# Optimization experiments

Measured on AMD Instinct MI355X. Metric: run time of the kernel, lower is better.

The kernel has to match this reference:

```python
import jax, jax.numpy as jnp
import numpy as np
import math

B, S, D, E, H = 8, 384, 768, 768, 12
HD = E // H
MAXL = 512

def _xavier(key, shape):
    fan_in, fan_out = shape[1], shape[0]
    lim = math.sqrt(6.0 / (fan_in + fan_out))
    return jax.random.uniform(key, shape, jnp.float32, -lim, lim)

def setup_inputs() -> dict:
    key = jax.random.key(0)
    ks = jax.random.split(key, 12)
    return {
        "x": jax.random.normal(ks[0], (B, S, D), jnp.float32),
        "mask": jnp.ones((B, S), jnp.int32),
        "segment_ids": jax.random.randint(ks[1], (B, S), 0, 2).astype(jnp.int32),
        "sep_distances": jax.random.normal(ks[2], (B, S), jnp.float32),
        "Wq": _xavier(ks[3], (E, D)), "bq": jnp.zeros((E,), jnp.float32),
        "Wk": _xavier(ks[4], (E, D)), "bk": jnp.zeros((E,), jnp.float32),
        "Wv": _xavier(ks[5], (E, D)), "bv": jnp.zeros((E,), jnp.float32),
        "rel_emb": jax.random.normal(ks[6], (2 * MAXL - 1, D), jnp.float32),
        "Wpk": _xavier(ks[7], (E, D)), "bpk": jnp.zeros((E,), jnp.float32),
        "Wpq": _xavier(ks[8], (E, D)), "bpq": jnp.zeros((E,), jnp.float32),
        "same_bias": jnp.zeros((H,), jnp.float32),
        "cross_bias": jnp.zeros((H,), jnp.float32),
        "sep_scale": jnp.full((H,), 0.25, jnp.float32),
        "sep_decay": jnp.full((H,), 0.35, jnp.float32),
        "Wo": _xavier(ks[9], (D, E)), "bo": jnp.zeros((D,), jnp.float32),
    }

def reference(x, mask, segment_ids, sep_distances, Wq, bq, Wk, bk, Wv, bv,
              rel_emb, Wpk, bpk, Wpq, bpq, same_bias, cross_bias,
              sep_scale, sep_decay, Wo, bo):
    b, s, _ = x.shape
    def shape_heads(t):  # [b,s,E] -> [b,H,s,HD]
        return t.reshape(b, s, H, HD).transpose(0, 2, 1, 3)
    q = shape_heads(x @ Wq.T + bq)
    k = shape_heads(x @ Wk.T + bk)
    v = shape_heads(x @ Wv.T + bv)
    # relative positions i - j, clamped and shifted
    rel_pos = jnp.arange(s)[:, None] - jnp.arange(s)[None, :]
    rel_pos = jnp.clip(rel_pos, -(MAXL - 1), MAXL - 1) + (MAXL - 1)
    rel = rel_emb[rel_pos]                     # [s,s,D]
    pos_k = (rel @ Wpk.T + bpk).reshape(s, s, H, HD)  # [i,j,h,d]
    pos_q = (rel @ Wpq.T + bpq).reshape(s, s, H, HD)
    c2c = jnp.einsum('bhid,bhjd->bhij', q, k)
    c2p = jnp.einsum('bhid,ijhd->bhij', q, pos_k)
    p2c = jnp.einsum('ijhd,bhjd->bhij', pos_q, k)
    logits = (c2c + c2p + p2c) / math.sqrt(HD * 3.0)
    # segment bias
    same = (segment_ids[:, :, None] == segment_ids[:, None, :]).astype(jnp.float32)[:, None]  # [b,1,s,s]
    cross = 1.0 - same
    hb = lambda p: p[None, :, None, None]
    seg_bias = same * hb(same_bias) + cross * hb(cross_bias)
    abs_sep = jnp.abs(sep_distances)
    gap = jnp.abs(abs_sep[:, :, None] - abs_sep[:, None, :])[:, None]  # [b,1,s,s]
    decay = jax.nn.softplus(sep_decay)[None, :, None, None] + 1e-4
    seg_bias = seg_bias + cross * jnp.exp(-gap * decay) * hb(sep_scale)
    logits = logits + seg_bias
    # mask: [b,s] -> [b,1,1,s]
    m = mask[:, None, None, :]
    logits = jnp.where(m == 0, jnp.float32(-9e15), logits)
    attn = jax.nn.softmax(logits, axis=-1)
    vals = jnp.einsum('bhij,bhjd->bhid', attn, v)
    vals = vals.transpose(0, 2, 1, 3).reshape(b, s, E)
    return vals @ Wo.T + bo
```

## Files before the change

### kernel.cpp

```cpp
#include <hip/hip_runtime.h>
#include <math.h>

#define B_  8
#define S_  384
#define H_  12
#define HD_ 64
#define E_  768
#define D_  768

typedef float  floatx4 __attribute__((ext_vector_type(4)));
typedef __bf16 bf16x8  __attribute__((ext_vector_type(8)));
typedef unsigned int ux4 __attribute__((ext_vector_type(4)));

__device__ __forceinline__ unsigned short f2bf(float f) {
    union { float f; unsigned u; } x; x.f = f;
    unsigned r = x.u + 0x7fff + ((x.u >> 16) & 1);
    return (unsigned short)(r >> 16);
}
__device__ __forceinline__ float bf2f(unsigned short u) {
    union { unsigned u; float f; } x; x.u = ((unsigned)u) << 16;
    return x.f;
}
__device__ __forceinline__ bf16x8 gld8(const unsigned short* p) {
    return __builtin_bit_cast(bf16x8, *(const ux4*)p);
}
__device__ __forceinline__ int tadr(int row, int cD) {
    return (row * 8 + (cD ^ (row & 7))) * 8;
}
__device__ __forceinline__ bf16x8 lds8(const unsigned short* base, int row, int cD) {
    return __builtin_bit_cast(bf16x8, *(const ux4*)(base + tadr(row, cD)));
}

__global__ __launch_bounds__(256) void convert_all(
    const float* __restrict__ x,
    const float* __restrict__ Wq, const float* __restrict__ Wk,
    const float* __restrict__ Wv, const float* __restrict__ Wo,
    const float* __restrict__ Wpk, const float* __restrict__ Wpq,
    const float* __restrict__ rel128,
    unsigned short* __restrict__ xb,
    unsigned short* __restrict__ wqb, unsigned short* __restrict__ wkb,
    unsigned short* __restrict__ wvb, unsigned short* __restrict__ wob,
    unsigned short* __restrict__ wpkb, unsigned short* __restrict__ wpqb,
    unsigned short* __restrict__ relb)
{
    const int seg = blockIdx.y;
    const int e = (blockIdx.x * 256 + threadIdx.x) * 4;
    const float* src;
    unsigned short* dst;
    if (seg < 4)       { src = x + (size_t)seg * 589824; dst = xb + (size_t)seg * 589824; }
    else if (seg == 4) { src = Wq;  dst = wqb; }
    else if (seg == 5) { src = Wk;  dst = wkb; }
    else if (seg == 6) { src = Wv;  dst = wvb; }
    else if (seg == 7) { src = Wo;  dst = wob; }
    else if (seg == 8) { src = Wpk; dst = wpkb; }
    else if (seg == 9) { src = Wpq; dst = wpqb; }
    else               { src = rel128; dst = relb; }

    float4 v;
    if (seg == 10 && e >= 767 * 768) v = make_float4(0.f, 0.f, 0.f, 0.f);
    else                             v = *(const float4*)(src + e);
    ushort4 o;
    o.x = f2bf(v.x); o.y = f2bf(v.y); o.z = f2bf(v.z); o.w = f2bf(v.w);
    *(ushort4*)(dst + e) = o;
}

__global__ __launch_bounds__(256) void proj_all(
    const unsigned short* __restrict__ xb, const unsigned short* __restrict__ relb,
    const unsigned short* __restrict__ wq, const unsigned short* __restrict__ wk,
    const unsigned short* __restrict__ wv, const unsigned short* __restrict__ wpk,
    const unsigned short* __restrict__ wpq,
    const float* __restrict__ bq, const float* __restrict__ bk,
    const float* __restrict__ bv, const float* __restrict__ bpk,
    const float* __restrict__ bpq,
    unsigned short* __restrict__ qb, unsigned short* __restrict__ kb,
    unsigned short* __restrict__ vtb, unsigned short* __restrict__ pkb,
    unsigned short* __restrict__ pqb)
{
    const int bid = blockIdx.x;
    int z, mt, nt;
    if (bid < 864) {
        z = bid / 288; const int r = bid - z * 288; mt = r / 6; nt = r - mt * 6;
    } else {
        const int r2 = bid - 864; z = 3 + r2 / 72;
        const int r = r2 % 72; mt = r / 6; nt = r - mt * 6;
    }
    const int m0 = mt * 64, n0 = nt * 128;

    const unsigned short* A = (z < 3) ? xb : relb;
    const unsigned short* W = (z == 0) ? wq : (z == 1) ? wk : (z == 2) ? wv
                            : (z == 3) ? wpk : wpq;
    const float* bias = (z == 0) ? bq : (z == 1) ? bk : (z == 2) ? bv
                      : (z == 3) ? bpk : bpq;
    unsigned short* C = (z == 0) ? qb : (z == 1) ? kb : (z == 2) ? vtb
                      : (z == 3) ? pkb : pqb;

    __shared__ unsigned short As[64 * 64];
    __shared__ unsigned short Ws[128 * 64];

    const int tid  = threadIdx.x;
    const int lane = tid & 63;
    const int wv_  = tid >> 6;
    const int quad = lane >> 4, l16 = lane & 15;

    floatx4 acc[4][2];
#pragma unroll
    for (int i = 0; i < 4; ++i)
#pragma unroll
        for (int j = 0; j < 2; ++j) acc[i][j] = (floatx4){0.f, 0.f, 0.f, 0.f};

    for (int k0 = 0; k0 < 768; k0 += 64) {
        __syncthreads();
#pragma unroll
        for (int r = 0; r < 2; ++r) {
            const int idx = tid + 256 * r;
            const int row = idx >> 3, cL = idx & 7, cD = cL ^ (row & 7);
            __builtin_amdgcn_global_load_lds(
                (__attribute__((address_space(1))) void*)(A + (size_t)(m0 + row) * 768 + k0 + cD * 8),
                (__attribute__((address_space(3))) void*)&As[idx * 8], 16, 0, 0);
        }
#pragma unroll
        for (int r = 0; r < 4; ++r) {
            const int idx = tid + 256 * r;
            const int row = idx >> 3, cL = idx & 7, cD = cL ^ (row & 7);
            __builtin_amdgcn_global_load_lds(
                (__attribute__((address_space(1))) void*)(W + (size_t)(n0 + row) * 768 + k0 + cD * 8),
                (__attribute__((address_space(3))) void*)&Ws[idx * 8], 16, 0, 0);
        }
        __syncthreads();

        bf16x8 a[4][2], b[2][2];
#pragma unroll
        for (int mi = 0; mi < 4; ++mi)
#pragma unroll
            for (int kc = 0; kc < 2; ++kc)
                a[mi][kc] = lds8(As, mi * 16 + l16, kc * 4 + quad);
#pragma unroll
        for (int ni = 0; ni < 2; ++ni)
#pragma unroll
            for (int kc = 0; kc < 2; ++kc)
                b[ni][kc] = lds8(Ws, wv_ * 32 + ni * 16 + l16, kc * 4 + quad);
#pragma unroll
        for (int mi = 0; mi < 4; ++mi)
#pragma unroll
            for (int ni = 0; ni < 2; ++ni)
#pragma unroll
                for (int kc = 0; kc < 2; ++kc)
                    acc[mi][ni] = __builtin_amdgcn_mfma_f32_16x16x32_bf16(
                        a[mi][kc], b[ni][kc], acc[mi][ni], 0, 0, 0);
    }

#pragma unroll
    for (int ni = 0; ni < 2; ++ni) {
        const int n = n0 + wv_ * 32 + ni * 16 + l16;
        const float bn = bias[n];
#pragma unroll
        for (int mi = 0; mi < 4; ++mi) {
            const int mbase = m0 + mi * 16 + quad * 4;
            if (z == 2) {
                const int bb = mbase / S_, s = mbase - bb * S_;
                const int h = n >> 6, hd = n & 63;
                ushort4 o;
                o.x = f2bf(acc[mi][ni][0] + bn);
                o.y = f2bf(acc[mi][ni][1] + bn);
                o.z = f2bf(acc[mi][ni][2] + bn);
                o.w = f2bf(acc[mi][ni][3] + bn);
                *(ushort4*)&C[(((size_t)(bb * H_ + h) << 6) + hd) * S_ + s] = o;
            } else if (z < 2) {
#pragma unroll
                for (int reg = 0; reg < 4; ++reg) {
                    const int m = mbase + reg;
                    const int bb = m / S_, s = m - bb * S_;
                    const int h = n >> 6, hd = n & 63;
                    C[(((size_t)(bb * H_ + h) * S_ + s) << 6) + hd] =
                        f2bf(acc[mi][ni][reg] + bn);
                }
            } else {
#pragma unroll
                for (int reg = 0; reg < 4; ++reg)
                    C[(size_t)(mbase + reg) * 768 + n] = f2bf(acc[mi][ni][reg] + bn);
            }
        }
    }
}

__global__ __launch_bounds__(256) void gemm_out(
    const unsigned short* __restrict__ A, const unsigned short* __restrict__ W,
    const float* __restrict__ bias, float* __restrict__ C)
{
    const int mt = blockIdx.x / 6, nt = blockIdx.x - mt * 6;
    const int m0 = mt * 64, n0 = nt * 128;

    __shared__ unsigned short As[64 * 64];
    __shared__ unsigned short Ws[128 * 64];

    const int tid  = threadIdx.x;
    const int lane = tid & 63;
    const int wv_  = tid >> 6;
    const int quad = lane >> 4, l16 = lane & 15;

    floatx4 acc[4][2];
#pragma unroll
    for (int i = 0; i < 4; ++i)
#pragma unroll
        for (int j = 0; j < 2; ++j) acc[i][j] = (floatx4){0.f, 0.f, 0.f, 0.f};

    for (int k0 = 0; k0 < 768; k0 += 64) {
        __syncthreads();
#pragma unroll
        for (int r = 0; r < 2; ++r) {
            const int idx = tid + 256 * r;
            const int row = idx >> 3, cL = idx & 7, cD = cL ^ (row & 7);
            __builtin_amdgcn_global_load_lds(
                (__attribute__((address_space(1))) void*)(A + (size_t)(m0 + row) * 768 + k0 + cD * 8),
                (__attribute__((address_space(3))) void*)&As[idx * 8], 16, 0, 0);
        }
#pragma unroll
        for (int r = 0; r < 4; ++r) {
            const int idx = tid + 256 * r;
            const int row = idx >> 3, cL = idx & 7, cD = cL ^ (row & 7);
            __builtin_amdgcn_global_load_lds(
                (__attribute__((address_space(1))) void*)(W + (size_t)(n0 + row) * 768 + k0 + cD * 8),
                (__attribute__((address_space(3))) void*)&Ws[idx * 8], 16, 0, 0);
        }
        __syncthreads();

        bf16x8 a[4][2], b[2][2];
#pragma unroll
        for (int mi = 0; mi < 4; ++mi)
#pragma unroll
            for (int kc = 0; kc < 2; ++kc)
                a[mi][kc] = lds8(As, mi * 16 + l16, kc * 4 + quad);
#pragma unroll
        for (int ni = 0; ni < 2; ++ni)
#pragma unroll
            for (int kc = 0; kc < 2; ++kc)
                b[ni][kc] = lds8(Ws, wv_ * 32 + ni * 16 + l16, kc * 4 + quad);
#pragma unroll
        for (int mi = 0; mi < 4; ++mi)
#pragma unroll
            for (int ni = 0; ni < 2; ++ni)
#pragma unroll
                for (int kc = 0; kc < 2; ++kc)
                    acc[mi][ni] = __builtin_amdgcn_mfma_f32_16x16x32_bf16(
                        a[mi][kc], b[ni][kc], acc[mi][ni], 0, 0, 0);
    }

#pragma unroll
    for (int ni = 0; ni < 2; ++ni) {
        const int n = n0 + wv_ * 32 + ni * 16 + l16;
        const float bn = bias[n];
#pragma unroll
        for (int mi = 0; mi < 4; ++mi)
#pragma unroll
            for (int reg = 0; reg < 4; ++reg) {
                const int m = m0 + mi * 16 + quad * 4 + reg;
                C[(size_t)m * 768 + n] = acc[mi][ni][reg] + bn;
            }
    }
}

__global__ __launch_bounds__(256) void attn_mfma(
    const unsigned short* __restrict__ qg, const unsigned short* __restrict__ kg,
    const unsigned short* __restrict__ vtg,
    const unsigned short* __restrict__ pkg, const unsigned short* __restrict__ pqg,
    const int* __restrict__ seg, const float* __restrict__ sep,
    const int* __restrict__ mask,
    const float* __restrict__ same_bias, const float* __restrict__ cross_bias,
    const float* __restrict__ sep_scale, const float* __restrict__ sep_decay,
    unsigned short* __restrict__ part_O, float* __restrict__ part_ml)
{
    __shared__ unsigned short Ks [64 * 64];
    __shared__ unsigned short Vts[64 * 64];
    __shared__ unsigned short PKs[128 * 64];
    __shared__ unsigned short PQs[128 * 64];
    __shared__ float CP[64 * 68];

    const int tid  = threadIdx.x;
    const int lane = tid & 63, w = tid >> 6;
    const int l16  = lane & 15, quad = lane >> 4;
    const int ty = tid >> 4, tx = tid & 15;
    const int it = blockIdx.x, h = blockIdx.y;
    const int b  = blockIdx.z / 6, jt = blockIdx.z - 6 * b;
    const int i0 = it * 64, j0 = jt * 64;
    const size_t bh = (size_t)(b * H_ + h);

    const unsigned short* kbase  = kg  + bh * S_ * 64;
    const unsigned short* vtbase = vtg + bh * 64 * S_;
    const int dbase = i0 - j0 + 320;

    bf16x8 qf[2];
#pragma unroll
    for (int ks = 0; ks < 2; ++ks)
        qf[ks] = gld8(qg + (bh * S_ + i0 + 16 * w + l16) * 64 + ks * 32 + quad * 8);

#pragma unroll
    for (int r = 0; r < 2; ++r) {
        const int idx = tid + 256 * r;
        const int row = idx >> 3, cL = idx & 7;
        const int cD = cL ^ (row & 7);
        __builtin_amdgcn_global_load_lds(
            (__attribute__((address_space(1))) void*)(kbase + (size_t)(j0 + row) * 64 + cD * 8),
            (__attribute__((address_space(3))) void*)&Ks[idx * 8], 16, 0, 0);
        __builtin_amdgcn_global_load_lds(
            (__attribute__((address_space(1))) void*)(vtbase + (size_t)row * S_ + j0 + cD * 8),
            (__attribute__((address_space(3))) void*)&Vts[idx * 8], 16, 0, 0);
    }
#pragma unroll
    for (int r = 0; r < 4; ++r) {
        const int idx = tid + 256 * r;
        const int row = idx >> 3, cL = idx & 7;
        const int cD = cL ^ (row & 7);
        const size_t go = (size_t)(dbase + row) * 768 + h * 64 + cD * 8;
        __builtin_amdgcn_global_load_lds(
            (__attribute__((address_space(1))) void*)(pkg + go),
            (__attribute__((address_space(3))) void*)&PKs[idx * 8], 16, 0, 0);
        __builtin_amdgcn_global_load_lds(
            (__attribute__((address_space(1))) void*)(pqg + go),
            (__attribute__((address_space(3))) void*)&PQs[idx * 8], 16, 0, 0);
    }

    float ai_r[4]; int si_r[4];
#pragma unroll
    for (int p = 0; p < 4; ++p) {
        const int ii = 4 * ty + p;
        ai_r[p] = fabsf(sep[b * S_ + i0 + ii]);
        si_r[p] = seg[b * S_ + i0 + ii];
    }

    const float sb  = same_bias[h];
    const float cb  = cross_bias[h];
    const float ssc = sep_scale[h];
    const float sd  = sep_decay[h];
    const float dec = fmaxf(sd, 0.f) + log1pf(__expf(-fabsf(sd))) + 1e-4f;
    const float isc = 0.07216878364870323f;

    __syncthreads();

    bf16x8 kf[4][2];
#pragma unroll
    for (int nj = 0; nj < 4; ++nj)
#pragma unroll
        for (int ks = 0; ks < 2; ++ks)
            kf[nj][ks] = lds8(Ks, 16 * nj + l16, ks * 4 + quad);

#pragma unroll
    for (int nj = 0; nj < 4; ++nj) {
        floatx4 acc = (floatx4){0.f, 0.f, 0.f, 0.f};
#pragma unroll
        for (int ks = 0; ks < 2; ++ks)
            acc = __builtin_amdgcn_mfma_f32_16x16x32_bf16(qf[ks], kf[nj][ks], acc, 0, 0, 0);
#pragma unroll
        for (int reg = 0; reg < 4; ++reg) {
            const int ii = 16 * w + quad * 4 + reg;
            CP[ii * 68 + 16 * nj + l16] = acc[reg];
        }
    }

#pragma unroll
    for (int f = 0; f < 5; ++f) {
        const int nd = w + f;
        floatx4 acc = (floatx4){0.f, 0.f, 0.f, 0.f};
#pragma unroll
        for (int ks = 0; ks < 2; ++ks) {
            bf16x8 bf = lds8(PKs, 16 * nd + l16, ks * 4 + quad);
            acc = __builtin_amdgcn_mfma_f32_16x16x32_bf16(qf[ks], bf, acc, 0, 0, 0);
        }
        const int ddloc = 16 * nd + l16;
#pragma unroll
        for (int reg = 0; reg < 4; ++reg) {
            const int ii = 16 * w + quad * 4 + reg;
            const int jj = ii - ddloc + 63;
            if (jj >= 0 && jj < 64)
                CP[ii * 68 + jj] += acc[reg];
        }
    }

#pragma unroll
    for (int f = 0; f < 5; ++f) {
        const int nd = w + f;
        bf16x8 pqf[2];
#pragma unroll
        for (int ks = 0; ks < 2; ++ks)
            pqf[ks] = lds8(PQs, 16 * nd + l16, ks * 4 + quad);
#pragma unroll
        for (int g = 0; g < 2; ++g) {
            const int nj = (g == 0) ? (3 - f) : (4 - f);
            if (nj < 0 || nj > 3) continue;
            floatx4 acc = (floatx4){0.f, 0.f, 0.f, 0.f};
#pragma unroll
            for (int ks = 0; ks < 2; ++ks)
                acc = __builtin_amdgcn_mfma_f32_16x16x32_bf16(pqf[ks], kf[nj][ks], acc, 0, 0, 0);
            const int jj = 16 * nj + l16;
#pragma unroll
            for (int reg = 0; reg < 4; ++reg) {
                const int ddloc = 16 * nd + quad * 4 + reg;
                const int ii = ddloc + jj - 63;
                if (ii >= 16 * w && ii < 16 * w + 16)
                    CP[ii * 68 + jj] += acc[reg];
            }
        }
    }

    unsigned short* Pp = (unsigned short*)CP;
    float* pml = part_ml + (size_t)(jt * 576 + ((b * H_ + h) * 6 + it)) * 128;
#pragma unroll
    for (int p = 0; p < 4; ++p) {
        const int ii = 4 * ty + p;
        const float aii = ai_r[p];
        const int   sii = si_r[p];
        float lg[4];
        float tmax = -INFINITY;
#pragma unroll
        for (int r = 0; r < 4; ++r) {
            const int jl = 4 * tx + r;
            float xv = CP[ii * 68 + jl] * isc;
            const float ajv = fabsf(sep[b * S_ + j0 + jl]);
            const int   sjv = seg[b * S_ + j0 + jl];
            const float gap = fabsf(aii - ajv);
            const float bias = (sii == sjv) ? sb
                             : cb + __expf(-gap * dec) * ssc;
            xv += bias;
            if (mask[b * S_ + j0 + jl] == 0) xv = -9.0e15f;
            lg[r] = xv;
            tmax = fmaxf(tmax, xv);
        }
#pragma unroll
        for (int off = 1; off < 16; off <<= 1)
            tmax = fmaxf(tmax, __shfl_xor(tmax, off));
        float rs = 0.f;
        ushort4 pw;
#pragma unroll
        for (int r = 0; r < 4; ++r) {
            const float e = __expf(lg[r] - tmax);
            rs += e;
            ((unsigned short*)&pw)[r] = f2bf(e);
        }
#pragma unroll
        for (int off = 1; off < 16; off <<= 1)
            rs += __shfl_xor(rs, off);
        if (tx == 0) {
            pml[ii]      = tmax;
            pml[64 + ii] = rs;
        }
        *(ushort4*)&Pp[ii * 136 + 4 * tx] = pw;
    }

    bf16x8 pA[2];
#pragma unroll
    for (int ks = 0; ks < 2; ++ks)
        pA[ks] = __builtin_bit_cast(bf16x8,
            *(const ux4*)&Pp[(16 * w + l16) * 136 + ks * 32 + quad * 8]);
    floatx4 O[4];
#pragma unroll
    for (int nd = 0; nd < 4; ++nd) {
        O[nd] = (floatx4){0.f, 0.f, 0.f, 0.f};
#pragma unroll
        for (int ks = 0; ks < 2; ++ks) {
            bf16x8 bf = lds8(Vts, 16 * nd + l16, ks * 4 + quad);
            O[nd] = __builtin_amdgcn_mfma_f32_16x16x32_bf16(pA[ks], bf, O[nd], 0, 0, 0);
        }
    }

    unsigned short* pO = part_O + (size_t)(jt * 576 + ((b * H_ + h) * 6 + it)) * 4096;
#pragma unroll
    for (int nd = 0; nd < 4; ++nd) {
        const int d = 16 * nd + l16;
#pragma unroll
        for (int reg = 0; reg < 4; ++reg) {
            const int ii = 16 * w + quad * 4 + reg;
            pO[ii * 64 + d] = f2bf(O[nd][reg]);
        }
    }
}

__global__ __launch_bounds__(256) void merge_attn(
    const unsigned short* __restrict__ part_O, const float* __restrict__ part_ml,
    unsigned short* __restrict__ vals)
{
    const int idx = blockIdx.x;
    const int b  = idx / (H_ * 6);
    const int r  = idx - b * H_ * 6;
    const int h  = r / 6, it = r - h * 6;
    const int tid = threadIdx.x;
    const int ii = tid >> 2, c = (tid & 3) * 16;

    float m[6], l[6];
#pragma unroll
    for (int jc = 0; jc < 6; ++jc) {
        const float* pml = part_ml + (size_t)(jc * 576 + idx) * 128;
        m[jc] = pml[ii];
        l[jc] = pml[64 + ii];
    }
    float M = m[0];
#pragma unroll
    for (int jc = 1; jc < 6; ++jc) M = fmaxf(M, m[jc]);
    float wsum = 0.f, wc[6];
#pragma unroll
    for (int jc = 0; jc < 6; ++jc) {
        wc[jc] = __expf(m[jc] - M);
        wsum += wc[jc] * l[jc];
    }
    const float inv = (wsum > 0.f) ? 1.f / wsum : 0.f;

    float o[16];
#pragma unroll
    for (int e = 0; e < 16; ++e) o[e] = 0.f;
#pragma unroll
    for (int jc = 0; jc < 6; ++jc) {
        const unsigned short* pO = part_O + ((size_t)(jc * 576 + idx)) * 4096
                                 + ii * 64 + c;
        ux4 u0 = *(const ux4*)pO;
        ux4 u1 = *(const ux4*)(pO + 8);
        const unsigned short* us0 = (const unsigned short*)&u0;
        const unsigned short* us1 = (const unsigned short*)&u1;
#pragma unroll
        for (int e = 0; e < 8; ++e) {
            o[e]     += wc[jc] * bf2f(us0[e]);
            o[8 + e] += wc[jc] * bf2f(us1[e]);
        }
    }
    ushort4 w0, w1, w2, w3;
#pragma unroll
    for (int e = 0; e < 4; ++e) {
        ((unsigned short*)&w0)[e] = f2bf(o[e] * inv);
        ((unsigned short*)&w1)[e] = f2bf(o[4 + e] * inv);
        ((unsigned short*)&w2)[e] = f2bf(o[8 + e] * inv);
        ((unsigned short*)&w3)[e] = f2bf(o[12 + e] * inv);
    }
    unsigned short* dst = vals + ((size_t)(b * S_ + it * 64 + ii)) * E_ + h * 64 + c;
    *(ushort4*)(dst)      = w0;
    *(ushort4*)(dst + 4)  = w1;
    *(ushort4*)(dst + 8)  = w2;
    *(ushort4*)(dst + 12) = w3;
}

extern "C" void kernel_launch(void* const* d_in, const int* in_sizes, int n_in,
                              void* d_out, int out_size, void* d_ws, size_t ws_size,
                              hipStream_t stream)
{
    const float* x         = (const float*)d_in[0];
    const int*   mask      = (const int*)d_in[1];
    const int*   seg       = (const int*)d_in[2];
    const float* sep       = (const float*)d_in[3];
    const float* Wq        = (const float*)d_in[4];
    const float* bq        = (const float*)d_in[5];
    const float* Wk        = (const float*)d_in[6];
    const float* bk        = (const float*)d_in[7];
    const float* Wv        = (const float*)d_in[8];
    const float* bv        = (const float*)d_in[9];
    const float* rel_emb   = (const float*)d_in[10];
    const float* Wpk       = (const float*)d_in[11];
    const float* bpk       = (const float*)d_in[12];
    const float* Wpq       = (const float*)d_in[13];
    const float* bpq       = (const float*)d_in[14];
    const float* same_bias = (const float*)d_in[15];
    const float* cross_bias= (const float*)d_in[16];
    const float* sep_scale = (const float*)d_in[17];
    const float* sep_decay = (const float*)d_in[18];
    const float* Wo        = (const float*)d_in[19];
    const float* bo        = (const float*)d_in[20];

    const size_t QKVN = (size_t)B_ * S_ * E_;
    const size_t WN   = (size_t)768 * 768;

    unsigned short* xb    = (unsigned short*)d_ws;
    unsigned short* wqb   = xb   + QKVN;
    unsigned short* wkb   = wqb  + WN;
    unsigned short* wvb   = wkb  + WN;
    unsigned short* wob   = wvb  + WN;
    unsigned short* wpkb  = wob  + WN;
    unsigned short* wpqb  = wpkb + WN;
    unsigned short* relb  = wpqb + WN;
    unsigned short* qb    = relb + WN;
    unsigned short* kb    = qb   + QKVN;
    unsigned short* vtb   = kb   + QKVN;
    unsigned short* pkb   = vtb  + QKVN;
    unsigned short* pqb   = pkb  + WN;
    unsigned short* valsb = pqb  + WN;
    unsigned short* partO = valsb + QKVN;
    float*          partml= (float*)(partO + (size_t)6 * 576 * 4096);

    convert_all<<<dim3(576, 11), 256, 0, stream>>>(
        x, Wq, Wk, Wv, Wo, Wpk, Wpq, rel_emb + (size_t)128 * D_,
        xb, wqb, wkb, wvb, wob, wpkb, wpqb, relb);

    proj_all<<<dim3(1008), 256, 0, stream>>>(
        xb, relb, wqb, wkb, wvb, wpkb, wpqb,
        bq, bk, bv, bpk, bpq, qb, kb, vtb, pkb, pqb);

    attn_mfma<<<dim3(6, 12, 48), 256, 0, stream>>>(
        qb, kb, vtb, pkb, pqb, seg, sep, mask,
        same_bias, cross_bias, sep_scale, sep_decay, partO, partml);

    merge_attn<<<dim3(576), 256, 0, stream>>>(partO, partml, valsb);

    gemm_out<<<dim3(288), 256, 0, stream>>>(valsb, wob, bo, (float*)d_out);
}
```

Before: 211.4 us.

## Load attention MFMA operands directly from global memory instead of staging in LDS

Drops the LDS staging buffers for K, V^T and the positional key/query tiles. MFMA fragments are now read straight from global memory, which also removes the block-wide barrier. The j-side sep, segment and mask values are loaded into registers once before the softmax loop, and the kernel asks for 4 blocks per CU via launch bounds. The aim is to cut LDS use and allow higher occupancy, at the cost of less coalesced and partly redundant global loads that depend on L1/L2 hits.

```diff
diff --git a/kernel.cpp b/kernel.cpp
--- a/kernel.cpp
+++ b/kernel.cpp
@@ -259,7 +259,7 @@
     }
 }
 
-__global__ __launch_bounds__(256) void attn_mfma(
+__global__ __launch_bounds__(256, 4) void attn_mfma(
     const unsigned short* __restrict__ qg, const unsigned short* __restrict__ kg,
     const unsigned short* __restrict__ vtg,
     const unsigned short* __restrict__ pkg, const unsigned short* __restrict__ pqg,
@@ -269,10 +269,6 @@
     const float* __restrict__ sep_scale, const float* __restrict__ sep_decay,
     unsigned short* __restrict__ part_O, float* __restrict__ part_ml)
 {
-    __shared__ unsigned short Ks [64 * 64];
-    __shared__ unsigned short Vts[64 * 64];
-    __shared__ unsigned short PKs[128 * 64];
-    __shared__ unsigned short PQs[128 * 64];
     __shared__ float CP[64 * 68];
 
     const int tid  = threadIdx.x;
@@ -293,31 +289,13 @@
     for (int ks = 0; ks < 2; ++ks)
         qf[ks] = gld8(qg + (bh * S_ + i0 + 16 * w + l16) * 64 + ks * 32 + quad * 8);
 
-#pragma unroll
-    for (int r = 0; r < 2; ++r) {
-        const int idx = tid + 256 * r;
-        const int row = idx >> 3, cL = idx & 7;
-        const int cD = cL ^ (row & 7);
-        __builtin_amdgcn_global_load_lds(
-            (__attribute__((address_space(1))) void*)(kbase + (size_t)(j0 + row) * 64 + cD * 8),
-            (__attribute__((address_space(3))) void*)&Ks[idx * 8], 16, 0, 0);
-        __builtin_amdgcn_global_load_lds(
-            (__attribute__((address_space(1))) void*)(vtbase + (size_t)row * S_ + j0 + cD * 8),
-            (__attribute__((address_space(3))) void*)&Vts[idx * 8], 16, 0, 0);
-    }
-#pragma unroll
-    for (int r = 0; r < 4; ++r) {
-        const int idx = tid + 256 * r;
-        const int row = idx >> 3, cL = idx & 7;
-        const int cD = cL ^ (row & 7);
-        const size_t go = (size_t)(dbase + row) * 768 + h * 64 + cD * 8;
-        __builtin_amdgcn_global_load_lds(
-            (__attribute__((address_space(1))) void*)(pkg + go),
-            (__attribute__((address_space(3))) void*)&PKs[idx * 8], 16, 0, 0);
-        __builtin_amdgcn_global_load_lds(
-            (__attribute__((address_space(1))) void*)(pqg + go),
-            (__attribute__((address_space(3))) void*)&PQs[idx * 8], 16, 0, 0);
-    }
+    bf16x8 kf[4][2];
+#pragma unroll
+    for (int nj = 0; nj < 4; ++nj)
+#pragma unroll
+        for (int ks = 0; ks < 2; ++ks)
+            kf[nj][ks] = gld8(kbase + (size_t)(j0 + 16 * nj + l16) * 64
+                              + ks * 32 + quad * 8);
 
     float ai_r[4]; int si_r[4];
 #pragma unroll
@@ -325,6 +303,14 @@
         const int ii = 4 * ty + p;
         ai_r[p] = fabsf(sep[b * S_ + i0 + ii]);
         si_r[p] = seg[b * S_ + i0 + ii];
+    }
+    float aj_r[4]; int sj_r[4], mk_r[4];
+#pragma unroll
+    for (int r = 0; r < 4; ++r) {
+        const int jl = 4 * tx + r;
+        aj_r[r] = fabsf(sep[b * S_ + j0 + jl]);
+        sj_r[r] = seg[b * S_ + j0 + jl];
+        mk_r[r] = mask[b * S_ + j0 + jl];
     }
 
     const float sb  = same_bias[h];
@@ -334,15 +320,6 @@
     const float dec = fmaxf(sd, 0.f) + log1pf(__expf(-fabsf(sd))) + 1e-4f;
     const float isc = 0.07216878364870323f;
 
-    __syncthreads();
-
-    bf16x8 kf[4][2];
-#pragma unroll
-    for (int nj = 0; nj < 4; ++nj)
-#pragma unroll
-        for (int ks = 0; ks < 2; ++ks)
-            kf[nj][ks] = lds8(Ks, 16 * nj + l16, ks * 4 + quad);
-
 #pragma unroll
     for (int nj = 0; nj < 4; ++nj) {
         floatx4 acc = (floatx4){0.f, 0.f, 0.f, 0.f};
@@ -362,7 +339,8 @@
         floatx4 acc = (floatx4){0.f, 0.f, 0.f, 0.f};
 #pragma unroll
         for (int ks = 0; ks < 2; ++ks) {
-            bf16x8 bf = lds8(PKs, 16 * nd + l16, ks * 4 + quad);
+            bf16x8 bf = gld8(pkg + (size_t)(dbase + 16 * nd + l16) * 768
+                             + h * 64 + ks * 32 + quad * 8);
             acc = __builtin_amdgcn_mfma_f32_16x16x32_bf16(qf[ks], bf, acc, 0, 0, 0);
         }
         const int ddloc = 16 * nd + l16;
@@ -381,7 +359,8 @@
         bf16x8 pqf[2];
 #pragma unroll
         for (int ks = 0; ks < 2; ++ks)
-            pqf[ks] = lds8(PQs, 16 * nd + l16, ks * 4 + quad);
+            pqf[ks] = gld8(pqg + (size_t)(dbase + 16 * nd + l16) * 768
+                           + h * 64 + ks * 32 + quad * 8);
 #pragma unroll
         for (int g = 0; g < 2; ++g) {
             const int nj = (g == 0) ? (3 - f) : (4 - f);
@@ -414,13 +393,11 @@
         for (int r = 0; r < 4; ++r) {
             const int jl = 4 * tx + r;
             float xv = CP[ii * 68 + jl] * isc;
-            const float ajv = fabsf(sep[b * S_ + j0 + jl]);
-            const int   sjv = seg[b * S_ + j0 + jl];
-            const float gap = fabsf(aii - ajv);
-            const float bias = (sii == sjv) ? sb
+            const float gap = fabsf(aii - aj_r[r]);
+            const float bias = (sii == sj_r[r]) ? sb
                              : cb + __expf(-gap * dec) * ssc;
             xv += bias;
-            if (mask[b * S_ + j0 + jl] == 0) xv = -9.0e15f;
+            if (mk_r[r] == 0) xv = -9.0e15f;
             lg[r] = xv;
             tmax = fmaxf(tmax, xv);
         }
@@ -456,7 +433,8 @@
         O[nd] = (floatx4){0.f, 0.f, 0.f, 0.f};
 #pragma unroll
         for (int ks = 0; ks < 2; ++ks) {
-            bf16x8 bf = lds8(Vts, 16 * nd + l16, ks * 4 + quad);
+            bf16x8 bf = gld8(vtbase + (size_t)(16 * nd + l16) * S_
+                             + j0 + ks * 32 + quad * 8);
             O[nd] = __builtin_amdgcn_mfma_f32_16x16x32_bf16(pA[ks], bf, O[nd], 0, 0, 0);
         }
     }
```

Result: slower. 218.6 us (+3.4%).
